# Kernel optimization log

Hardware: AMD Instinct MI355X
Metric: run time of the kernel (lower is better)

Reference implementation:

```python
import jax, jax.numpy as jnp
import numpy as np

B, T, D = 32, 1024, 1024
K, F = 8, 4096
E, RH = 64, 128
NUM_STAGES, NUM_VIEWS = 5, 4


def setup_inputs() -> dict:
    key = jax.random.key(0)
    ks = jax.random.split(key, 16)
    s = 0.02
    return {
        "x": jax.random.normal(ks[0], (B, T, D), dtype=jnp.float32),
        "stage_ids": jax.random.randint(ks[1], (B,), 0, NUM_STAGES),
        "view_ids": jax.random.randint(ks[2], (B,), 0, NUM_VIEWS),
        # router params
        "stage_emb": jax.random.normal(ks[3], (NUM_STAGES, E), dtype=jnp.float32) * s,
        "view_emb": jax.random.normal(ks[4], (NUM_VIEWS, E), dtype=jnp.float32) * s,
        "rw1": jax.random.normal(ks[5], (2 * E, RH), dtype=jnp.float32) * s,
        "rb1": jnp.zeros((RH,), dtype=jnp.float32),
        "rw2": jax.random.normal(ks[6], (RH, K), dtype=jnp.float32) * s,
        "rb2": jnp.zeros((K,), dtype=jnp.float32),
        # stacked expert FFN params
        "w1": jax.random.normal(ks[7], (K, D, F), dtype=jnp.float32) * s,
        "b1": jnp.zeros((K, F), dtype=jnp.float32),
        "w2": jax.random.normal(ks[8], (K, F, D), dtype=jnp.float32) * s,
        "b2": jnp.zeros((K, D), dtype=jnp.float32),
    }


def _moe_forward(x, stage_ids, view_ids, stage_emb, view_emb, rw1, rb1, rw2, rb2, w1, b1, w2, b2):
    # Router: per-sample stage/view embeddings -> MLP -> softmax over experts
    z = jnp.concatenate([stage_emb[stage_ids], view_emb[view_ids]], axis=-1)  # [B, 2E]
    logits = jax.nn.relu(z @ rw1 + rb1) @ rw2 + rb2  # [B, K]
    expert_probs = jax.nn.softmax(logits, axis=-1)
    selected_expert = jnp.argmax(expert_probs, axis=-1)  # [B]

    # Top-1 dispatch: gather the selected expert's weights per sample, then
    # run a single batched FFN (equivalent math to per-expert masked loop).
    w1s = w1[selected_expert]  # [B, D, F]
    b1s = b1[selected_expert]  # [B, F]
    w2s = w2[selected_expert]  # [B, F, D]
    b2s = b2[selected_expert]  # [B, D]
    h = jax.nn.gelu(jnp.einsum('btd,bdf->btf', x, w1s) + b1s[:, None, :], approximate=False)
    output = jnp.einsum('btf,bfd->btd', h, w2s) + b2s[:, None, :]  # [B, T, D]

    # Switch-style load-balance loss: K * sum_i f_i * P_i
    expert_mask = jax.nn.one_hot(selected_expert, K, dtype=jnp.float32)  # [B, K]
    f = expert_mask.mean(axis=0)
    P = expert_probs.mean(axis=0)
    load_balance_loss = K * jnp.sum(f * P)
    return output, expert_probs, selected_expert, load_balance_loss


def reference(x, stage_ids, view_ids, stage_emb, view_emb, rw1, rb1, rw2, rb2, w1, b1, w2, b2):
    return _moe_forward(x, stage_ids, view_ids, stage_emb, view_emb, rw1, rb1, rw2, rb2, w1, b1, w2, b2)
```

## Files before the change

### kernel.cpp

```cpp
#include <hip/hip_runtime.h>
#include <hip/hip_bf16.h>
#include <math.h>

#define BATCH 32
#define TSEQ 1024
#define DMODEL 1024
#define KEXP 8
#define FFFN 4096
#define EEMB 64
#define RHID 128
#define NSTAGE 5
#define NVIEW 4

typedef float f32x4 __attribute__((ext_vector_type(4)));
typedef __bf16 bf16x8 __attribute__((ext_vector_type(8)));

#define AS1C(p) ((const __attribute__((address_space(1))) unsigned int*)(p))
#define AS3(p)  ((__attribute__((address_space(3))) unsigned int*)(p))

__device__ __forceinline__ unsigned short f32_to_bf16_rne(float f) {
    union { float f; unsigned int u; } v; v.f = f;
    unsigned int u = v.u;
    unsigned int r = u + 0x7FFFu + ((u >> 16) & 1u);
    return (unsigned short)(r >> 16);
}

__device__ void resolve_ids_r18(const int* __restrict__ raw, int* __restrict__ out, int hi) {
    bool is64 = true;
    for (int i = 1; i < 32; i += 2) is64 = is64 && (raw[i] == 0);
    for (int i = 0; i < 32; i += 2) is64 = is64 && (raw[i] >= 0 && raw[i] < hi);
    for (int b = 0; b < BATCH; ++b) {
        int v = is64 ? raw[2 * b] : raw[b];
        v = v < 0 ? 0 : (v >= hi ? hi - 1 : v);
        out[b] = v;
    }
}

__global__ __launch_bounds__(512) void router_r18(
    const int* __restrict__ stage_ids,
    const int* __restrict__ view_ids,
    const float* __restrict__ stage_emb,
    const float* __restrict__ view_emb,
    const float* __restrict__ rw1,
    const float* __restrict__ rb1,
    const float* __restrict__ rw2,
    const float* __restrict__ rb2,
    float* __restrict__ out_probs,
    float* __restrict__ out_sel,
    float* __restrict__ out_loss,
    int* __restrict__ sel_ws)
{
    __shared__ int sids[BATCH], vids[BATCH];
    __shared__ double z[4][2 * EEMB];
    __shared__ double h[4][RHID];
    __shared__ double lg[4][KEXP];
    __shared__ double Psum[4][KEXP];
    __shared__ int fcount[4][KEXP];
    const int t = threadIdx.x;
    const int g = t >> 7;
    const int u = t & 127;
    if (t == 0) {
        resolve_ids_r18(stage_ids, sids, NSTAGE);
        resolve_ids_r18(view_ids, vids, NVIEW);
    }
    if (u < KEXP) { Psum[g][u] = 0.0; fcount[g][u] = 0; }
    __syncthreads();

    for (int b0 = 0; b0 < BATCH; b0 += 4) {
        const int b = b0 + g;
        const int sid = sids[b], vid = vids[b];
        z[g][u] = (u < EEMB) ? (double)stage_emb[sid * EEMB + u]
                             : (double)view_emb[vid * EEMB + (u - EEMB)];
        __syncthreads();
        double acc = (double)rb1[u];
        for (int i = 0; i < 2 * EEMB; ++i) acc += z[g][i] * (double)rw1[i * RHID + u];
        h[g][u] = fmax(acc, 0.0);
        __syncthreads();
        if (u < KEXP) {
            double a = (double)rb2[u];
            for (int i = 0; i < RHID; ++i) a += h[g][i] * (double)rw2[i * KEXP + u];
            lg[g][u] = a;
        }
        __syncthreads();
        if (u == 0) {
            double mx = lg[g][0]; int am = 0;
            for (int k = 1; k < KEXP; ++k) if (lg[g][k] > mx) { mx = lg[g][k]; am = k; }
            double p[KEXP]; double den = 0.0;
            for (int k = 0; k < KEXP; ++k) { p[k] = exp(lg[g][k] - mx); den += p[k]; }
            for (int k = 0; k < KEXP; ++k) {
                double pk = p[k] / den;
                out_probs[b * KEXP + k] = (float)pk;
                Psum[g][k] += pk;
            }
            out_sel[b] = (float)am;
            sel_ws[b] = am;
            fcount[g][am] += 1;
        }
        __syncthreads();
    }
    if (t == 0) {
        double loss = 0.0;
        for (int k = 0; k < KEXP; ++k) {
            double ps = Psum[0][k] + Psum[1][k] + Psum[2][k] + Psum[3][k];
            int fc = fcount[0][k] + fcount[1][k] + fcount[2][k] + fcount[3][k];
            loss += ((double)fc / (double)BATCH) * (ps / (double)BATCH);
        }
        out_loss[0] = (float)((double)KEXP * loss);
    }
}

__global__ void cvt_f32_bf16_r18(const float* __restrict__ src,
                                 unsigned short* __restrict__ dst, size_t n)
{
    size_t i = (size_t)blockIdx.x * blockDim.x + threadIdx.x;
    size_t stride = (size_t)gridDim.x * blockDim.x;
    for (size_t j = i * 4; j < n; j += stride * 4) {
        float4 v = *(const float4*)(src + j);
        ushort4 o;
        o.x = f32_to_bf16_rne(v.x); o.y = f32_to_bf16_rne(v.y);
        o.z = f32_to_bf16_rne(v.z); o.w = f32_to_bf16_rne(v.w);
        *(ushort4*)(dst + j) = o;
    }
}

__global__ __launch_bounds__(512) void transpose_f32_bf16_r18(
    const float* __restrict__ src, unsigned short* __restrict__ dst, int R, int C)
{
    __shared__ float tile[64][65];
    const int e = blockIdx.z;
    const float* s = src + (size_t)e * R * C;
    unsigned short* d = dst + (size_t)e * R * C;
    const int c0 = blockIdx.x * 64, r0 = blockIdx.y * 64;
    const int tx = threadIdx.x, ty = threadIdx.y;
    #pragma unroll
    for (int i = 0; i < 64; i += 8)
        tile[ty + i][tx] = s[(size_t)(r0 + ty + i) * C + (c0 + tx)];
    __syncthreads();
    #pragma unroll
    for (int i = 0; i < 64; i += 8)
        d[(size_t)(c0 + ty + i) * R + (r0 + tx)] = f32_to_bf16_rne(tile[tx][ty + i]);
}


#define BM 128
#define BN 128
#define BK 64

template<int MODE, int OBF>
__global__ __launch_bounds__(256, 2) void gemm_bt_r18(
    const unsigned short* __restrict__ Aall,
    const unsigned short* __restrict__ BTall,
    const float* __restrict__ biasAll,
    void* __restrict__ OutV,
    const int* __restrict__ sel, int g0,
    int M, int N, int K)
{
    const int bz = blockIdx.z;
    int e = sel[g0 + bz];
    e = e < 0 ? 0 : (e >= KEXP ? KEXP - 1 : e);
    const unsigned short* A  = Aall + (size_t)bz * M * K;
    const unsigned short* BT = BTall + (size_t)e * (size_t)N * K;
    const float* bias = biasAll + (size_t)e * N;

    __shared__ __align__(16) unsigned short As[BM][BK];
    __shared__ __align__(16) unsigned short Bs[BN][BK];

    const int tid  = threadIdx.x;
    const int lane = tid & 63;
    const int wave = tid >> 6;
    const int wr = wave >> 1;
    const int wc = wave & 1;
    const int fr = lane & 15;
    const int fq = lane >> 4;
    const int swz = fr & 7;

    const int brow = blockIdx.y * BM;
    const int bcol = blockIdx.x * BN;

    const int srow = lane >> 3;
    const int scol = ((lane & 7) ^ (lane >> 3)) * 8;

    const f32x4 zero = {0.f, 0.f, 0.f, 0.f};
    f32x4 acc[4][4];
    #pragma unroll
    for (int m = 0; m < 4; ++m)
        #pragma unroll
        for (int n = 0; n < 4; ++n) acc[m][n] = zero;

    for (int k0 = 0; k0 < K; k0 += BK) {
        #pragma unroll
        for (int i = 0; i < 4; ++i) {
            const int r0 = i * 32 + wave * 8;
            const unsigned short* gA = A + (size_t)(brow + r0 + srow) * K + (k0 + scol);
            __builtin_amdgcn_global_load_lds(AS1C(gA), AS3(&As[r0][0]), 16, 0, 0);
        }
        #pragma unroll
        for (int i = 0; i < 4; ++i) {
            const int r0 = i * 32 + wave * 8;
            const unsigned short* gB = BT + (size_t)(bcol + r0 + srow) * K + (k0 + scol);
            __builtin_amdgcn_global_load_lds(AS1C(gB), AS3(&Bs[r0][0]), 16, 0, 0);
        }
        __syncthreads();

        bf16x8 af[4][2], bfr[4][2];
        #pragma unroll
        for (int m = 0; m < 4; ++m) {
            const int ra = wr * 64 + m * 16 + fr;
            #pragma unroll
            for (int ks = 0; ks < 2; ++ks) {
                const int ch = (ks * 4 + fq) ^ swz;
                af[m][ks] = *(const bf16x8*)(&As[ra][ch * 8]);
            }
        }
        #pragma unroll
        for (int n = 0; n < 4; ++n) {
            const int rb = wc * 64 + n * 16 + fr;
            #pragma unroll
            for (int ks = 0; ks < 2; ++ks) {
                const int ch = (ks * 4 + fq) ^ swz;
                bfr[n][ks] = *(const bf16x8*)(&Bs[rb][ch * 8]);
            }
        }

        #pragma unroll
        for (int ks = 0; ks < 2; ++ks)
            #pragma unroll
            for (int m = 0; m < 4; ++m)
                #pragma unroll
                for (int n = 0; n < 4; ++n)
                    acc[m][n] = __builtin_amdgcn_mfma_f32_16x16x32_bf16(af[m][ks], bfr[n][ks], acc[m][n], 0, 0, 0);

        __syncthreads();
    }

    #pragma unroll
    for (int m = 0; m < 4; ++m) {
        #pragma unroll
        for (int n = 0; n < 4; ++n) {
            #pragma unroll
            for (int r = 0; r < 4; ++r) {
                const int row = brow + wr * 64 + m * 16 + fq * 4 + r;
                const int col = bcol + wc * 64 + n * 16 + fr;
                float v = acc[m][n][r] + bias[col];
                if (MODE == 0) v = 0.5f * v * (1.0f + erff(v * 0.70710678118654752f));
                const size_t idx = (size_t)bz * M * N + (size_t)row * N + col;
                if (OBF) ((unsigned short*)OutV)[idx] = f32_to_bf16_rne(v);
                else     ((float*)OutV)[idx] = v;
            }
        }
    }
}

extern "C" void kernel_launch(void* const* d_in, const int* in_sizes, int n_in,
                              void* d_out, int out_size, void* d_ws, size_t ws_size,
                              hipStream_t stream)
{
    const float* x         = (const float*)d_in[0];
    const int*   stage_ids = (const int*)d_in[1];
    const int*   view_ids  = (const int*)d_in[2];
    const float* stage_emb = (const float*)d_in[3];
    const float* view_emb  = (const float*)d_in[4];
    const float* rw1       = (const float*)d_in[5];
    const float* rb1       = (const float*)d_in[6];
    const float* rw2       = (const float*)d_in[7];
    const float* rb2       = (const float*)d_in[8];
    const float* w1        = (const float*)d_in[9];
    const float* b1        = (const float*)d_in[10];
    const float* w2        = (const float*)d_in[11];
    const float* b2        = (const float*)d_in[12];

    float* out_f = (float*)d_out;
    const size_t OUT_ELEMS = (size_t)BATCH * TSEQ * DMODEL;

    const size_t MB64 = 67108864ull;
    char* ws = (char*)d_ws;
    int* sel_ws            = (int*)ws;
    unsigned short* x_bf   = (unsigned short*)(ws + 4096);
    unsigned short* w1T    = (unsigned short*)(ws + 4096 + MB64);
    unsigned short* w2T    = (unsigned short*)(ws + 4096 + 2 * MB64);
    unsigned short* h_bf   = (unsigned short*)(ws + 4096 + 3 * MB64);

    int grp = 1;
    {
        const size_t base = 4096 + 3 * MB64;
        const size_t avail = ws_size > base ? ws_size - base : 0;
        for (int g = 32; g >= 1; g >>= 1) {
            if ((size_t)g * TSEQ * FFFN * 2 <= avail) { grp = g; break; }
        }
    }

    router_r18<<<1, 512, 0, stream>>>(stage_ids, view_ids, stage_emb, view_emb,
        rw1, rb1, rw2, rb2,
        out_f + OUT_ELEMS,
        out_f + OUT_ELEMS + BATCH * KEXP,
        out_f + OUT_ELEMS + BATCH * KEXP + BATCH,
        sel_ws);

    cvt_f32_bf16_r18<<<2048, 256, 0, stream>>>(x, x_bf, (size_t)BATCH * TSEQ * DMODEL);
    dim3 tb(64, 8);
    transpose_f32_bf16_r18<<<dim3(FFFN / 64, DMODEL / 64, KEXP), tb, 0, stream>>>(w1, w1T, DMODEL, FFFN);
    transpose_f32_bf16_r18<<<dim3(DMODEL / 64, FFFN / 64, KEXP), tb, 0, stream>>>(w2, w2T, FFFN, DMODEL);

    for (int g0 = 0; g0 < BATCH; g0 += grp) {
        gemm_bt_r18<0, 1><<<dim3(FFFN / BN, TSEQ / BM, grp), 256, 0, stream>>>(
            x_bf + (size_t)g0 * TSEQ * DMODEL, w1T, b1,
            (void*)h_bf, sel_ws, g0, TSEQ, FFFN, DMODEL);
        gemm_bt_r18<1, 0><<<dim3(DMODEL / BN, TSEQ / BM, grp), 256, 0, stream>>>(
            h_bf, w2T, b2,
            (void*)(out_f + (size_t)g0 * TSEQ * DMODEL), sel_ws, g0, TSEQ, DMODEL, FFFN);
    }
}
```

Before: 893.1 us.

## Enlarge GEMM M-tile to 256 and stream A fragments per k-step

```diff
diff --git a/kernel.cpp b/kernel.cpp
--- a/kernel.cpp
+++ b/kernel.cpp
@@ -25,7 +25,7 @@
     return (unsigned short)(r >> 16);
 }
 
-__device__ void resolve_ids_r18(const int* __restrict__ raw, int* __restrict__ out, int hi) {
+__device__ void resolve_ids_r20(const int* __restrict__ raw, int* __restrict__ out, int hi) {
     bool is64 = true;
     for (int i = 1; i < 32; i += 2) is64 = is64 && (raw[i] == 0);
     for (int i = 0; i < 32; i += 2) is64 = is64 && (raw[i] >= 0 && raw[i] < hi);
@@ -36,7 +36,7 @@
     }
 }
 
-__global__ __launch_bounds__(512) void router_r18(
+__global__ __launch_bounds__(512) void router_r20(
     const int* __restrict__ stage_ids,
     const int* __restrict__ view_ids,
     const float* __restrict__ stage_emb,
@@ -60,8 +60,8 @@
     const int g = t >> 7;
     const int u = t & 127;
     if (t == 0) {
-        resolve_ids_r18(stage_ids, sids, NSTAGE);
-        resolve_ids_r18(view_ids, vids, NVIEW);
+        resolve_ids_r20(stage_ids, sids, NSTAGE);
+        resolve_ids_r20(view_ids, vids, NVIEW);
     }
     if (u < KEXP) { Psum[g][u] = 0.0; fcount[g][u] = 0; }
     __syncthreads();
@@ -109,7 +109,7 @@
     }
 }
 
-__global__ void cvt_f32_bf16_r18(const float* __restrict__ src,
+__global__ void cvt_f32_bf16_r20(const float* __restrict__ src,
                                  unsigned short* __restrict__ dst, size_t n)
 {
     size_t i = (size_t)blockIdx.x * blockDim.x + threadIdx.x;
@@ -123,7 +123,7 @@
     }
 }
 
-__global__ __launch_bounds__(512) void transpose_f32_bf16_r18(
+__global__ __launch_bounds__(512) void transpose_f32_bf16_r20(
     const float* __restrict__ src, unsigned short* __restrict__ dst, int R, int C)
 {
     __shared__ float tile[64][65];
@@ -142,12 +142,12 @@
 }
 
 
-#define BM 128
+#define BM 256
 #define BN 128
 #define BK 64
 
 template<int MODE, int OBF>
-__global__ __launch_bounds__(256, 2) void gemm_bt_r18(
+__global__ __launch_bounds__(256, 2) void gemm_bt_r20(
     const unsigned short* __restrict__ Aall,
     const unsigned short* __restrict__ BTall,
     const float* __restrict__ biasAll,
@@ -181,15 +181,15 @@
     const int scol = ((lane & 7) ^ (lane >> 3)) * 8;
 
     const f32x4 zero = {0.f, 0.f, 0.f, 0.f};
-    f32x4 acc[4][4];
+    f32x4 acc[8][4];
     #pragma unroll
-    for (int m = 0; m < 4; ++m)
+    for (int m = 0; m < 8; ++m)
         #pragma unroll
         for (int n = 0; n < 4; ++n) acc[m][n] = zero;
 
     for (int k0 = 0; k0 < K; k0 += BK) {
         #pragma unroll
-        for (int i = 0; i < 4; ++i) {
+        for (int i = 0; i < 8; ++i) {
             const int r0 = i * 32 + wave * 8;
             const unsigned short* gA = A + (size_t)(brow + r0 + srow) * K + (k0 + scol);
             __builtin_amdgcn_global_load_lds(AS1C(gA), AS3(&As[r0][0]), 16, 0, 0);
@@ -202,44 +202,35 @@
         }
         __syncthreads();
 
-        bf16x8 af[4][2], bfr[4][2];
-        #pragma unroll
-        for (int m = 0; m < 4; ++m) {
-            const int ra = wr * 64 + m * 16 + fr;
+        #pragma unroll
+        for (int ks = 0; ks < 2; ++ks) {
+            const int ch = ((ks * 4 + fq) ^ swz) * 8;
+            bf16x8 bfr[4];
             #pragma unroll
-            for (int ks = 0; ks < 2; ++ks) {
-                const int ch = (ks * 4 + fq) ^ swz;
-                af[m][ks] = *(const bf16x8*)(&As[ra][ch * 8]);
+            for (int n = 0; n < 4; ++n) {
+                const int rb = wc * 64 + n * 16 + fr;
+                bfr[n] = *(const bf16x8*)(&Bs[rb][ch]);
             }
-        }
-        #pragma unroll
-        for (int n = 0; n < 4; ++n) {
-            const int rb = wc * 64 + n * 16 + fr;
             #pragma unroll
-            for (int ks = 0; ks < 2; ++ks) {
-                const int ch = (ks * 4 + fq) ^ swz;
-                bfr[n][ks] = *(const bf16x8*)(&Bs[rb][ch * 8]);
-            }
-        }
-
-        #pragma unroll
-        for (int ks = 0; ks < 2; ++ks)
-            #pragma unroll
-            for (int m = 0; m < 4; ++m)
+            for (int m = 0; m < 8; ++m) {
+                const int ra = wr * 128 + m * 16 + fr;
+                const bf16x8 af = *(const bf16x8*)(&As[ra][ch]);
                 #pragma unroll
                 for (int n = 0; n < 4; ++n)
-                    acc[m][n] = __builtin_amdgcn_mfma_f32_16x16x32_bf16(af[m][ks], bfr[n][ks], acc[m][n], 0, 0, 0);
+                    acc[m][n] = __builtin_amdgcn_mfma_f32_16x16x32_bf16(af, bfr[n], acc[m][n], 0, 0, 0);
+            }
+        }
 
         __syncthreads();
     }
 
     #pragma unroll
-    for (int m = 0; m < 4; ++m) {
+    for (int m = 0; m < 8; ++m) {
         #pragma unroll
         for (int n = 0; n < 4; ++n) {
             #pragma unroll
             for (int r = 0; r < 4; ++r) {
-                const int row = brow + wr * 64 + m * 16 + fq * 4 + r;
+                const int row = brow + wr * 128 + m * 16 + fq * 4 + r;
                 const int col = bcol + wc * 64 + n * 16 + fr;
                 float v = acc[m][n][r] + bias[col];
                 if (MODE == 0) v = 0.5f * v * (1.0f + erff(v * 0.70710678118654752f));
@@ -289,23 +280,23 @@
         }
     }
 
-    router_r18<<<1, 512, 0, stream>>>(stage_ids, view_ids, stage_emb, view_emb,
+    router_r20<<<1, 512, 0, stream>>>(stage_ids, view_ids, stage_emb, view_emb,
         rw1, rb1, rw2, rb2,
         out_f + OUT_ELEMS,
         out_f + OUT_ELEMS + BATCH * KEXP,
         out_f + OUT_ELEMS + BATCH * KEXP + BATCH,
         sel_ws);
 
-    cvt_f32_bf16_r18<<<2048, 256, 0, stream>>>(x, x_bf, (size_t)BATCH * TSEQ * DMODEL);
+    cvt_f32_bf16_r20<<<2048, 256, 0, stream>>>(x, x_bf, (size_t)BATCH * TSEQ * DMODEL);
     dim3 tb(64, 8);
-    transpose_f32_bf16_r18<<<dim3(FFFN / 64, DMODEL / 64, KEXP), tb, 0, stream>>>(w1, w1T, DMODEL, FFFN);
-    transpose_f32_bf16_r18<<<dim3(DMODEL / 64, FFFN / 64, KEXP), tb, 0, stream>>>(w2, w2T, FFFN, DMODEL);
+    transpose_f32_bf16_r20<<<dim3(FFFN / 64, DMODEL / 64, KEXP), tb, 0, stream>>>(w1, w1T, DMODEL, FFFN);
+    transpose_f32_bf16_r20<<<dim3(DMODEL / 64, FFFN / 64, KEXP), tb, 0, stream>>>(w2, w2T, FFFN, DMODEL);
 
     for (int g0 = 0; g0 < BATCH; g0 += grp) {
-        gemm_bt_r18<0, 1><<<dim3(FFFN / BN, TSEQ / BM, grp), 256, 0, stream>>>(
+        gemm_bt_r20<0, 1><<<dim3(FFFN / BN, TSEQ / BM, grp), 256, 0, stream>>>(
             x_bf + (size_t)g0 * TSEQ * DMODEL, w1T, b1,
             (void*)h_bf, sel_ws, g0, TSEQ, FFFN, DMODEL);
-        gemm_bt_r18<1, 0><<<dim3(DMODEL / BN, TSEQ / BM, grp), 256, 0, stream>>>(
+        gemm_bt_r20<1, 0><<<dim3(DMODEL / BN, TSEQ / BM, grp), 256, 0, stream>>>(
             h_bf, w2T, b2,
             (void*)(out_f + (size_t)g0 * TSEQ * DMODEL), sel_ws, g0, TSEQ, DMODEL, FFFN);
     }
```

After: 933.9 us. 1.05x slower.
